# Optimization experiments

Hardware: AMD Instinct MI355X
Metric: run time of the kernel (lower is better)

Reference implementation:

```python
import jax, jax.numpy as jnp
import numpy as np

N = 50000      # nodes
E = 800000     # edges
T = 3          # npass
ED = 64        # embedding_dim
NS = 23        # nshifts (arange(0.8, 3.0+1e-5, 0.1))
MD = NS + ED   # message_dim = 87
H = 200        # hidden width (hardcoded in module)
NMOL = 2048    # number of molecules (segments for final scatter)
RD = ED * (T + 1)  # readout input dim = 256
EPS = 1e-5

SHIFTS = jnp.asarray(np.arange(0.8, 3.0 + 1e-5, 0.1, dtype=np.float32))  # [23]


def setup_inputs() -> dict:
    key = jax.random.key(0)
    ks = jax.random.split(key, 32)
    inp = {
        'z_i': jax.random.randint(ks[0], (N,), 0, 10),
        'edge_index': jax.random.randint(ks[1], (2, E), 0, N),
        'dist_ij': jax.random.uniform(ks[2], (E, 1), dtype=jnp.float32) * 2.2 + 0.8,
        'mol_ind': jnp.sort(jax.random.randint(ks[3], (N,), 0, NMOL)),
        'emb': jax.random.normal(ks[4], (10, ED), dtype=jnp.float32),
        # per-pass update MLP params, stacked over T
        'up_bn_g': jnp.ones((T, MD), jnp.float32),
        'up_bn_b': jnp.zeros((T, MD), jnp.float32),
        'up_w1': jax.random.normal(ks[5], (T, MD, H), jnp.float32) * 0.05,
        'up_b1': jnp.zeros((T, H), jnp.float32),
        'up_w2': jax.random.normal(ks[6], (T, H, H), jnp.float32) * 0.05,
        'up_b2': jnp.zeros((T, H), jnp.float32),
        'up_w3': jax.random.normal(ks[7], (T, H, H), jnp.float32) * 0.05,
        'up_b3': jnp.zeros((T, H), jnp.float32),
        'up_w4': jax.random.normal(ks[8], (T, H, ED), jnp.float32) * 0.05,
        'up_b4': jnp.zeros((T, ED), jnp.float32),
        # readout MLP params
        'ro_bn_g': jnp.ones((RD,), jnp.float32),
        'ro_bn_b': jnp.zeros((RD,), jnp.float32),
        'ro_w1': jax.random.normal(ks[9], (RD, H), jnp.float32) * 0.05,
        'ro_b1': jnp.zeros((H,), jnp.float32),
        'ro_w2': jax.random.normal(ks[10], (H, H), jnp.float32) * 0.05,
        'ro_b2': jnp.zeros((H,), jnp.float32),
        'ro_w3': jax.random.normal(ks[11], (H, H), jnp.float32) * 0.05,
        'ro_b3': jnp.zeros((H,), jnp.float32),
        'ro_w4': jax.random.normal(ks[12], (H, 1), jnp.float32) * 0.05,
        'ro_b4': jnp.zeros((1,), jnp.float32),  # bias filled to 0 in __init__
    }
    return inp


def batchnorm(x, g, b):
    # BatchNorm1d in training mode: batch statistics, biased variance
    mu = jnp.mean(x, axis=0)
    var = jnp.mean(jnp.square(x - mu), axis=0)
    return (x - mu) * jax.lax.rsqrt(var + EPS) * g + b


def mlp(x, g, b, w1, b1, w2, b2, w3, b3, w4, b4):
    x = batchnorm(x, g, b)
    x = jax.nn.relu(x @ w1 + b1)
    x = jax.nn.relu(x @ w2 + b2)
    x = jax.nn.relu(x @ w3 + b3)
    return x @ w4 + b4


def reference(z_i, edge_index, dist_ij, mol_ind, emb,
              up_bn_g, up_bn_b, up_w1, up_b1, up_w2, up_b2, up_w3, up_b3, up_w4, up_b4,
              ro_bn_g, ro_bn_b, ro_w1, ro_b1, ro_w2, ro_b2, ro_w3, ro_b3, ro_w4, ro_b4):
    e_source, e_sink = edge_index[0], edge_index[1]
    rbf_ij = jnp.exp(-jnp.square(dist_ij - SHIFTS[None, :]))  # [E, NS]
    x_i = emb[z_i]                                            # [N, ED]
    x_list = [x_i]
    for t in range(T):
        m_ij = jnp.concatenate([rbf_ij, x_i[e_sink]], axis=1)  # [E, MD] gather
        m_i = jax.ops.segment_sum(m_ij, e_source, num_segments=N)  # scatter-sum
        x_i = x_i + 0.1 * mlp(m_i, up_bn_g[t], up_bn_b[t],
                              up_w1[t], up_b1[t], up_w2[t], up_b2[t],
                              up_w3[t], up_b3[t], up_w4[t], up_b4[t])
        x_list.append(x_i)
    x_all = jnp.concatenate(x_list, axis=1)  # [N, RD]
    y_i = mlp(x_all, ro_bn_g, ro_bn_b, ro_w1, ro_b1, ro_w2, ro_b2, ro_w3, ro_b3, ro_w4, ro_b4)
    y = jax.ops.segment_sum(y_i, mol_ind, num_segments=NMOL)  # [NMOL, 1]
    return y
```

## Files before the change

### kernel.cpp

```cpp
#include <hip/hip_runtime.h>
#include <hip/hip_bf16.h>
#include <type_traits>

#define NN 50000
#define NP 50048
#define EE 800000
#define TT 3
#define ED 64
#define NS 23
#define MD 87
#define HH 200
#define NMOL 2048
#define RD 256

#define SW 216
#define NPB2 512
#define SNB ((NN + 255) / 256)

typedef __attribute__((ext_vector_type(8))) short short8b;
typedef __attribute__((ext_vector_type(4))) float f32x4;

template <int V> using ic = std::integral_constant<int, V>;

__device__ __forceinline__ unsigned short f2bf(float f) {
  unsigned u = __float_as_uint(f);
  return (unsigned short)((u + 0x7fffu + ((u >> 16) & 1u)) >> 16);
}
__device__ __forceinline__ float ubf2f(unsigned short h) {
  return __uint_as_float(((unsigned)h) << 16);
}
__device__ __forceinline__ float bfp2f(unsigned p) {
  return __uint_as_float(p << 16) + __uint_as_float(p & 0xffff0000u);
}
__device__ __forceinline__ unsigned packsplit(float v) {
  unsigned short h = f2bf(v);
  unsigned short l = f2bf(v - ubf2f(h));
  return (unsigned)h | ((unsigned)l << 16);
}

struct WD { const float* src; short* dst; int K, N, Kpad, Npad, T; };
struct WDs { WD d[5]; };

__global__ __launch_bounds__(256) void wprep_kernel(WDs W) {
  WD w = W.d[blockIdx.y];
  int KB = w.Kpad >> 5, NT = w.Npad >> 4;
  int per = w.Npad * w.Kpad;
  int total = w.T * per;
  for (int idx = blockIdx.x * 256 + threadIdx.x; idx < total; idx += gridDim.x * 256) {
    int t = idx / per;
    int r = idx - t * per;
    int e = r & 7, lane = (r >> 3) & 63;
    int blk = r >> 9;
    int kb = blk % KB, tile = blk / KB;
    int ln = lane & 15, quad = lane >> 4;
    int n = tile * 16 + ln, k = kb * 32 + quad * 8 + e;
    float v = 0.f;
    if (k < w.K && n < w.N) v = w.src[((size_t)t * w.K + k) * w.N + n];
    unsigned short h = f2bf(v);
    unsigned short l = f2bf(v - ubf2f(h));
    size_t base = ((size_t)(t * NT + tile) * KB + kb) * 1024;
    w.dst[base + lane * 8 + e] = (short)h;
    w.dst[base + 512 + lane * 8 + e] = (short)l;
  }
}

__global__ __launch_bounds__(256) void wscale_kernel(const float* __restrict__ wsrc,
                                                     const float* __restrict__ na,
                                                     const float* __restrict__ nb,
                                                     const float* __restrict__ bsrc,
                                                     int K, int Kpad,
                                                     short* __restrict__ wsp,
                                                     float* __restrict__ bc) {
  int n = blockIdx.x;
  int k = threadIdx.x;
  int KB = Kpad >> 5;
  int tile = n >> 4, ln = n & 15;
  float contrib = 0.f;
  if (k < Kpad) {
    float v = 0.f;
    if (n < HH && k < K) {
      float w = wsrc[(size_t)k * HH + n];
      v = na[k] * w;
      contrib = nb[k] * w;
    }
    unsigned short h = f2bf(v);
    unsigned short l = f2bf(v - ubf2f(h));
    int kb = k >> 5, quad = (k & 31) >> 3, e = k & 7;
    int lane = quad * 16 + ln;
    size_t base = ((size_t)tile * KB + kb) * 1024;
    wsp[base + lane * 8 + e] = (short)h;
    wsp[base + 512 + lane * 8 + e] = (short)l;
  }
  __shared__ float sh[256];
  sh[k] = contrib;
  __syncthreads();
  for (int off = 128; off > 0; off >>= 1) {
    if (k < off) sh[k] += sh[k + off];
    __syncthreads();
  }
  if (k == 0) bc[n] = (n < HH ? bsrc[n] : 0.f) + sh[0];
}

__global__ __launch_bounds__(256) void emb_kernel(const int* __restrict__ z,
                                                  const float* __restrict__ emb,
                                                  unsigned* __restrict__ xp,
                                                  short* __restrict__ xq,
                                                  short* __restrict__ xqs) {
  int idx = blockIdx.x * 256 + threadIdx.x;
  if (idx >= NN * ED) return;
  int i = idx >> 6, d = idx & 63;
  unsigned pk = packsplit(emb[z[i] * ED + d]);
  xp[(size_t)i * RD + d] = pk;
  short h = (short)(pk & 0xffffu);
  xq[(size_t)i * RD + d] = h;
  xqs[(size_t)i * ED + d] = h;
}

__global__ __launch_bounds__(256) void hist_kernel(const int* __restrict__ src,
                                                   int* __restrict__ deg) {
  int e = blockIdx.x * 256 + threadIdx.x;
  if (e < EE) atomicAdd(&deg[src[e]], 1);
}

__global__ __launch_bounds__(256) void scanA_kernel(const int* __restrict__ deg,
                                                    int* __restrict__ Psum) {
  int i = blockIdx.x * 256 + threadIdx.x;
  int v = (i < NN) ? deg[i] : 0;
#pragma unroll
  for (int off = 32; off > 0; off >>= 1) v += __shfl_down(v, off, 64);
  __shared__ int ws[4];
  if ((threadIdx.x & 63) == 0) ws[threadIdx.x >> 6] = v;
  __syncthreads();
  if (threadIdx.x == 0) Psum[blockIdx.x] = ws[0] + ws[1] + ws[2] + ws[3];
}

__global__ __launch_bounds__(256) void scanB_kernel(const int* __restrict__ Psum,
                                                    int* __restrict__ Poff) {
  __shared__ int sh[256];
  int t = threadIdx.x;
  int v = (t < SNB) ? Psum[t] : 0;
  sh[t] = v;
  __syncthreads();
  for (int off = 1; off < 256; off <<= 1) {
    int u = (t >= off) ? sh[t - off] : 0;
    __syncthreads();
    sh[t] += u;
    __syncthreads();
  }
  if (t < SNB) Poff[t] = sh[t] - v;
}

__global__ __launch_bounds__(256) void scanC_kernel(const int* __restrict__ deg,
                                                    const int* __restrict__ Poff,
                                                    int* __restrict__ offs,
                                                    int* __restrict__ cursor) {
  __shared__ int sh[256];
  int t = threadIdx.x;
  int i = blockIdx.x * 256 + t;
  int v = (i < NN) ? deg[i] : 0;
  sh[t] = v;
  __syncthreads();
  for (int off = 1; off < 256; off <<= 1) {
    int u = (t >= off) ? sh[t - off] : 0;
    __syncthreads();
    sh[t] += u;
    __syncthreads();
  }
  int excl = Poff[blockIdx.x] + sh[t] - v;
  if (i < NN) {
    offs[i] = excl;
    cursor[i] = excl;
    if (i == NN - 1) offs[NN] = excl + v;
  }
}

__global__ __launch_bounds__(256) void scatter_kernel(const int* __restrict__ src,
                                                      const int* __restrict__ snk,
                                                      const float* __restrict__ dist,
                                                      int* __restrict__ cursor,
                                                      int* __restrict__ ssink,
                                                      float* __restrict__ sdist) {
  int e = blockIdx.x * 256 + threadIdx.x;
  if (e >= EE) return;
  int p = atomicAdd(&cursor[src[e]], 1);
  ssink[p] = snk[e];
  sdist[p] = dist[e];
}

template <bool RBF>
__global__ __launch_bounds__(256) void gather_kernel(const int* __restrict__ offs,
                                                     const int* __restrict__ ssink,
                                                     const float* __restrict__ sdist,
                                                     const short* __restrict__ xqs,
                                                     short* __restrict__ mh) {
  int node = blockIdx.x * 4 + (threadIdx.x >> 6);
  int lane = threadIdx.x & 63;
  if (node >= NN) return;
  float shift = (float)(0.8 + 0.1 * (double)lane);
  int e0 = offs[node], e1 = offs[node + 1];
  float ax0 = 0.f, ax1 = 0.f, ar0 = 0.f, ar1 = 0.f;
  int j = e0;
  for (; j + 4 <= e1; j += 4) {
    int s0 = ssink[j], s1 = ssink[j + 1], s2 = ssink[j + 2], s3 = ssink[j + 3];
    float x0 = ubf2f((unsigned short)xqs[(size_t)s0 * ED + lane]);
    float x1 = ubf2f((unsigned short)xqs[(size_t)s1 * ED + lane]);
    float x2 = ubf2f((unsigned short)xqs[(size_t)s2 * ED + lane]);
    float x3 = ubf2f((unsigned short)xqs[(size_t)s3 * ED + lane]);
    ax0 += x0 + x2;
    ax1 += x1 + x3;
    if (RBF && lane < NS) {
      float d0 = sdist[j], d1 = sdist[j + 1], d2 = sdist[j + 2], d3 = sdist[j + 3];
      float u0 = d0 - shift, u1 = d1 - shift, u2 = d2 - shift, u3 = d3 - shift;
      ar0 += __expf(-u0 * u0) + __expf(-u2 * u2);
      ar1 += __expf(-u1 * u1) + __expf(-u3 * u3);
    }
  }
  for (; j < e1; j++) {
    int s = ssink[j];
    ax0 += ubf2f((unsigned short)xqs[(size_t)s * ED + lane]);
    if (RBF && lane < NS) {
      float u = sdist[j] - shift;
      ar0 += __expf(-u * u);
    }
  }
  float accx = ax0 + ax1;
  if (RBF && lane < NS) mh[(size_t)node * 96 + lane] = (short)f2bf(ar0 + ar1);
  if (RBF && lane >= NS && lane < 32) mh[(size_t)node * 96 + 64 + lane] = 0;
  mh[(size_t)node * 96 + NS + lane] = (short)f2bf(accx);
}

template <int LD>
__global__ __launch_bounds__(256) void colstats_s16_kernel(const short* __restrict__ X,
                                                           float* __restrict__ P) {
  constexpr int CG = LD / 8;
  constexpr int RPB = 256 / CG;
  const int t = threadIdx.x;
  const int cg = t % CG, rin = t / CG;
  float s[8] = {0, 0, 0, 0, 0, 0, 0, 0}, q[8] = {0, 0, 0, 0, 0, 0, 0, 0};
  if (rin < RPB) {
    for (int r = blockIdx.x * RPB + rin; r < NN; r += gridDim.x * RPB) {
      union { uint4 v; short e[8]; } u;
      u.v = *(const uint4*)(X + (size_t)r * LD + cg * 8);
#pragma unroll
      for (int e = 0; e < 8; e++) {
        float f = ubf2f((unsigned short)u.e[e]);
        s[e] += f;
        q[e] += f * f;
      }
    }
  }
  __shared__ float sh[256][16];
#pragma unroll
  for (int e = 0; e < 8; e++) { sh[t][e] = s[e]; sh[t][8 + e] = q[e]; }
  __syncthreads();
  if (rin == 0) {
    for (int rr = 1; rr < RPB; rr++) {
      const float* o = sh[rr * CG + cg];
#pragma unroll
      for (int e = 0; e < 8; e++) { s[e] += o[e]; q[e] += o[8 + e]; }
    }
    float* Pb = P + blockIdx.x * 512;
#pragma unroll
    for (int e = 0; e < 8; e++) {
      Pb[cg * 8 + e] = s[e];
      Pb[256 + cg * 8 + e] = q[e];
    }
  }
}

__global__ __launch_bounds__(256) void bnfinal2_kernel(const float* __restrict__ P, int nblk,
                                                       const float* __restrict__ g,
                                                       const float* __restrict__ b, int ncols,
                                                       float* __restrict__ na,
                                                       float* __restrict__ nb) {
  int c = blockIdx.x;
  int t = threadIdx.x;
  float s = 0.f, q = 0.f;
  for (int i = t; i < nblk; i += 256) {
    s += P[i * 512 + c];
    q += P[i * 512 + 256 + c];
  }
#pragma unroll
  for (int off = 32; off > 0; off >>= 1) {
    s += __shfl_down(s, off, 64);
    q += __shfl_down(q, off, 64);
  }
  __shared__ float ws[4], wq[4];
  if ((t & 63) == 0) { ws[t >> 6] = s; wq[t >> 6] = q; }
  __syncthreads();
  if (t == 0) {
    s = ws[0] + ws[1] + ws[2] + ws[3];
    q = wq[0] + wq[1] + wq[2] + wq[3];
    if (c < ncols) {
      float mean = s / (float)NN;
      float var = q / (float)NN - mean * mean;
      float a = g[c] * rsqrtf(var + 1e-5f);
      na[c] = a;
      nb[c] = b[c] - mean * a;
    } else {
      na[c] = 0.f;
      nb[c] = 0.f;
    }
  }
}

template <bool READOUT>
__global__ __launch_bounds__(256, 2) void fused_kernel(
    const short* __restrict__ Agh,
    const short* __restrict__ W1p, const short* __restrict__ W2p,
    const short* __restrict__ W3p, const short* __restrict__ W4p,
    const float* __restrict__ b1, const float* __restrict__ b2,
    const float* __restrict__ b3, const float* __restrict__ b4,
    unsigned* __restrict__ xp, short* __restrict__ xq, short* __restrict__ xqs,
    int t, const float* __restrict__ w4ro, const int* __restrict__ mol,
    float* __restrict__ out) {
  __shared__ short act[64 * SW];
  constexpr int GLDA = READOUT ? RD : 96;
  constexpr int KB1 = READOUT ? 8 : 3;
  constexpr int NB = READOUT ? 32 : 28;
  const int tid = threadIdx.x;
  const int wave = tid >> 6, lane = tid & 63, ln = lane & 15, quad = lane >> 4;
  const int q8 = quad * 8;
  const int bm = blockIdx.x * 64;

  *(unsigned*)(act + (tid >> 2) * SW + 208 + (tid & 3) * 2) = 0u;

  f32x4 acc[4][4];
  short8b Breg[NB];
  const short8b zfrag = {0, 0, 0, 0, 0, 0, 0, 0};

  auto loadB = [&](auto slt, auto tmt, auto ntt, const short* __restrict__ Wp,
                   int KBfull, int kb0) {
    constexpr int SL = decltype(slt)::value;
    constexpr int TM = decltype(tmt)::value;
    constexpr int NT = decltype(ntt)::value;
#pragma unroll
    for (int j = 0; j < 4; j++) {
      int tile = wave + 4 * j;
      if (tile < NT) {
#pragma unroll
        for (int s = 0; s < SL; s++) {
          int kb = kb0 + ((TM == 2) ? (s >> 1) : s);
          int pl = (TM == 2) ? ((s & 1) << 9) : 0;
          Breg[j * SL + s] = *(const short8b*)(
              Wp + (size_t)(tile * KBfull + kb) * 1024 + pl + lane * 8);
        }
      }
    }
    __builtin_amdgcn_sched_barrier(0);
  };

  auto mfmaloop = [&](auto slt, auto tmt, auto ntt, auto gat, auto rstt, int kb0) {
    constexpr int SL = decltype(slt)::value;
    constexpr int TM = decltype(tmt)::value;
    constexpr int NT = decltype(ntt)::value;
    constexpr bool GA = decltype(gat)::value;
    constexpr bool RST = decltype(rstt)::value;
    constexpr int KB = SL / TM;
    if constexpr (RST) {
#pragma unroll
      for (int j = 0; j < 4; j++)
#pragma unroll
        for (int i = 0; i < 4; i++) acc[j][i] = (f32x4){0.f, 0.f, 0.f, 0.f};
    }
#pragma unroll
    for (int kb = 0; kb < KB; kb++) {
      int col = (kb0 + kb) * 32 + q8;
      short8b a[4];
#pragma unroll
      for (int i = 0; i < 4; i++) {
        if constexpr (GA)
          a[i] = __builtin_nontemporal_load(
              (const short8b*)(Agh + (size_t)(bm + i * 16 + ln) * GLDA + col));
        else
          a[i] = (col < 216) ? *(const short8b*)(act + (i * 16 + ln) * SW + col)
                             : zfrag;
      }
#pragma unroll
      for (int s2 = 0; s2 < TM; s2++)
#pragma unroll
        for (int j = 0; j < 4; j++) {
          int tile = wave + 4 * j;
          if (tile < NT) {
#pragma unroll
            for (int i = 0; i < 4; i++)
              acc[j][i] = __builtin_amdgcn_mfma_f32_16x16x32_bf16(
                  a[i], Breg[j * SL + kb * TM + s2], acc[j][i], 0, 0, 0);
          }
        }
    }
  };

  auto epi = [&](const float* __restrict__ bias) {
#pragma unroll
    for (int j = 0; j < 4; j++) {
      int tile = wave + 4 * j;
      if (tile < 13) {
        int colg = tile * 16 + ln;
        float bb = (colg < HH) ? bias[colg] : 0.f;
#pragma unroll
        for (int i = 0; i < 4; i++)
#pragma unroll
          for (int r = 0; r < 4; r++)
            act[(i * 16 + quad * 4 + r) * SW + colg] =
                (short)f2bf(fmaxf(acc[j][i][r] + bb, 0.f));
      }
    }
  };

  auto bar = [] {
    __builtin_amdgcn_sched_barrier(0);
    __builtin_amdgcn_s_barrier();
    __builtin_amdgcn_sched_barrier(0);
  };
  auto lgkmbar = [] {
    asm volatile("s_waitcnt lgkmcnt(0)" ::: "memory");
    __builtin_amdgcn_sched_barrier(0);
    __builtin_amdgcn_s_barrier();
    __builtin_amdgcn_sched_barrier(0);
  };

  using T = std::true_type;
  using F = std::false_type;

  if constexpr (!READOUT) {
    loadB(ic<6>{}, ic<2>{}, ic<13>{}, W1p, KB1, 0);
    mfmaloop(ic<6>{}, ic<2>{}, ic<13>{}, T{}, T{}, 0);
  } else {
    loadB(ic<8>{}, ic<2>{}, ic<13>{}, W1p, KB1, 0);
    mfmaloop(ic<8>{}, ic<2>{}, ic<13>{}, T{}, T{}, 0);
    loadB(ic<8>{}, ic<2>{}, ic<13>{}, W1p, KB1, 4);
    mfmaloop(ic<8>{}, ic<2>{}, ic<13>{}, T{}, F{}, 4);
  }
  loadB(ic<7>{}, ic<1>{}, ic<13>{}, W2p, 7, 0);
  epi(b1);
  lgkmbar();

  mfmaloop(ic<7>{}, ic<1>{}, ic<13>{}, F{}, T{}, 0);
  loadB(ic<7>{}, ic<1>{}, ic<13>{}, W3p, 7, 0);
  bar();
  epi(b2);
  lgkmbar();

  mfmaloop(ic<7>{}, ic<1>{}, ic<13>{}, F{}, T{}, 0);
  if constexpr (!READOUT)
    loadB(ic<14>{}, ic<2>{}, ic<4>{}, W4p, 7, 0);
  bar();
  epi(b3);
  lgkmbar();

  if constexpr (!READOUT) {
    mfmaloop(ic<14>{}, ic<2>{}, ic<4>{}, F{}, T{}, 0);
    int colg = wave * 16 + ln;
    float bb = b4[colg];
#pragma unroll
    for (int i = 0; i < 4; i++)
#pragma unroll
      for (int r = 0; r < 4; r++) {
        int grow = bm + i * 16 + quad * 4 + r;
        if (grow < NN) {
          size_t base = (size_t)grow * RD;
          float oldv = bfp2f(xp[base + (size_t)t * ED + colg]);
          unsigned pk = packsplit(oldv + 0.1f * (acc[0][i][r] + bb));
          xp[base + (size_t)(t + 1) * ED + colg] = pk;
          short h = (short)(pk & 0xffffu);
          xq[base + (size_t)(t + 1) * ED + colg] = h;
          xqs[(size_t)(t + 1) * NN * ED + (size_t)grow * ED + colg] = h;
        }
      }
  } else {
    int row = tid >> 2;
    float s = 0.f;
    for (int c = (tid & 3); c < HH; c += 4)
      s += ubf2f((unsigned short)act[row * SW + c]) * w4ro[c];
    s += __shfl_xor(s, 1, 64);
    s += __shfl_xor(s, 2, 64);
    int grow = bm + row;
    if ((tid & 3) == 0 && grow < NN) atomicAdd(&out[mol[grow]], s + b4[0]);
  }
}

extern "C" void kernel_launch(void* const* d_in, const int* in_sizes, int n_in,
                              void* d_out, int out_size, void* d_ws, size_t ws_size,
                              hipStream_t stream) {
  const int* z_i = (const int*)d_in[0];
  const int* e_src = (const int*)d_in[1];
  const int* e_snk = ((const int*)d_in[1]) + EE;
  const float* dist = (const float*)d_in[2];
  const int* mol = (const int*)d_in[3];
  const float* emb = (const float*)d_in[4];
  const float* up_bn_g = (const float*)d_in[5];
  const float* up_bn_b = (const float*)d_in[6];
  const float* up_w1 = (const float*)d_in[7];
  const float* up_b1 = (const float*)d_in[8];
  const float* up_w2 = (const float*)d_in[9];
  const float* up_b2 = (const float*)d_in[10];
  const float* up_w3 = (const float*)d_in[11];
  const float* up_b3 = (const float*)d_in[12];
  const float* up_w4 = (const float*)d_in[13];
  const float* up_b4 = (const float*)d_in[14];
  const float* ro_bn_g = (const float*)d_in[15];
  const float* ro_bn_b = (const float*)d_in[16];
  const float* ro_w1 = (const float*)d_in[17];
  const float* ro_b1 = (const float*)d_in[18];
  const float* ro_w2 = (const float*)d_in[19];
  const float* ro_b2 = (const float*)d_in[20];
  const float* ro_w3 = (const float*)d_in[21];
  const float* ro_b3 = (const float*)d_in[22];
  const float* ro_w4 = (const float*)d_in[23];
  const float* ro_b4 = (const float*)d_in[24];
  float* out = (float*)d_out;

  char* p = (char*)d_ws;
  auto alloc = [&](size_t bytes) {
    void* r = (void*)p;
    p += (bytes + 255) & ~(size_t)255;
    return r;
  };
  unsigned* x_p = (unsigned*)alloc((size_t)NN * RD * 4);
  short* x_q = (short*)alloc((size_t)NP * RD * 2);
  short* x_qs = (short*)alloc((size_t)(TT + 1) * NN * ED * 2);
  short* mh = (short*)alloc((size_t)NP * 96 * 2);
  int* ssink = (int*)alloc((size_t)EE * 4);
  float* sdist = (float*)alloc((size_t)EE * 4);
  int* offs = (int*)alloc((size_t)(NN + 1) * 4);
  int* deg = (int*)alloc((size_t)NN * 4);
  int* cursor = (int*)alloc((size_t)NN * 4);
  int* Psum = (int*)alloc((size_t)SNB * 4);
  int* Poff = (int*)alloc((size_t)SNB * 4);
  float* P = (float*)alloc((size_t)NPB2 * 512 * 4);
  float* na = (float*)alloc(256 * 4);
  float* nb = (float*)alloc(256 * 4);
  float* b1c = (float*)alloc(208 * 4);
  short* w1sp = (short*)alloc((size_t)13 * 3 * 1024 * 2);
  short* r1sp = (short*)alloc((size_t)13 * 8 * 1024 * 2);
  short* w2p = (short*)alloc((size_t)TT * 13 * 7 * 1024 * 2);
  short* w3p = (short*)alloc((size_t)TT * 13 * 7 * 1024 * 2);
  short* w4p = (short*)alloc((size_t)TT * 4 * 7 * 1024 * 2);
  short* r2p = (short*)alloc((size_t)13 * 7 * 1024 * 2);
  short* r3p = (short*)alloc((size_t)13 * 7 * 1024 * 2);

  hipMemsetAsync(deg, 0, (size_t)NN * 4, stream);
  hipMemsetAsync(out, 0, (size_t)NMOL * 4, stream);

  WDs descs;
  descs.d[0] = {up_w2, w2p, HH, HH, 224, 208, TT};
  descs.d[1] = {up_w3, w3p, HH, HH, 224, 208, TT};
  descs.d[2] = {up_w4, w4p, HH, ED, 224, 64, TT};
  descs.d[3] = {ro_w2, r2p, HH, HH, 224, 208, 1};
  descs.d[4] = {ro_w3, r3p, HH, HH, 224, 208, 1};
  wprep_kernel<<<dim3(546, 5), 256, 0, stream>>>(descs);

  emb_kernel<<<(NN * ED + 255) / 256, 256, 0, stream>>>(z_i, emb, x_p, x_q, x_qs);
  hist_kernel<<<(EE + 255) / 256, 256, 0, stream>>>(e_src, deg);
  scanA_kernel<<<SNB, 256, 0, stream>>>(deg, Psum);
  scanB_kernel<<<1, 256, 0, stream>>>(Psum, Poff);
  scanC_kernel<<<SNB, 256, 0, stream>>>(deg, Poff, offs, cursor);
  scatter_kernel<<<(EE + 255) / 256, 256, 0, stream>>>(e_src, e_snk, dist, cursor, ssink, sdist);

  const int gM = NP / 64;

  for (int t = 0; t < TT; t++) {
    if (t == 0)
      gather_kernel<true><<<(NN + 3) / 4, 256, 0, stream>>>(
          offs, ssink, sdist, x_qs, mh);
    else
      gather_kernel<false><<<(NN + 3) / 4, 256, 0, stream>>>(
          offs, ssink, sdist, x_qs + (size_t)t * NN * ED, mh);
    colstats_s16_kernel<96><<<NPB2, 256, 0, stream>>>(mh, P);
    bnfinal2_kernel<<<256, 256, 0, stream>>>(P, NPB2, up_bn_g + t * MD, up_bn_b + t * MD, MD,
                                             na, nb);
    wscale_kernel<<<208, 256, 0, stream>>>(up_w1 + (size_t)t * MD * HH, na, nb,
                                           up_b1 + t * HH, MD, 96, w1sp, b1c);
    fused_kernel<false><<<gM, 256, 0, stream>>>(
        mh, w1sp,
        w2p + (size_t)t * 13 * 7 * 1024, w3p + (size_t)t * 13 * 7 * 1024,
        w4p + (size_t)t * 4 * 7 * 1024,
        b1c, up_b2 + t * HH, up_b3 + t * HH, up_b4 + t * ED,
        x_p, x_q, x_qs, t, nullptr, nullptr, nullptr);
  }

  colstats_s16_kernel<256><<<NPB2, 256, 0, stream>>>(x_q, P);
  bnfinal2_kernel<<<256, 256, 0, stream>>>(P, NPB2, ro_bn_g, ro_bn_b, RD, na, nb);
  wscale_kernel<<<208, 256, 0, stream>>>(ro_w1, na, nb, ro_b1, RD, 256, r1sp, b1c);
  fused_kernel<true><<<gM, 256, 0, stream>>>(
      x_q, r1sp, r2p, r3p, nullptr,
      b1c, ro_b2, ro_b3, ro_b4,
      nullptr, nullptr, nullptr, 0, ro_w4, mol, out);

  (void)in_sizes; (void)n_in; (void)out_size; (void)ws_size;
}
```

Baseline: 555.0 us.

## Fuse batchnorm column statistics into producer kernels and drop separate stats passes

Column sum and sum-of-squares for the batchnorm inputs are now accumulated inside the gather, embedding, and fused MLP kernels via shared-memory reductions and global atomics. The mean/scale computation is folded into the weight-scaling kernel, which removes the colstats and bnfinal kernels and their extra reads of the message and feature matrices. The gather and embedding kernels become grid-stride with a fixed grid size. In exchange, the change adds atomic contention, per-pass memsets, and float-atomic ordering nondeterminism in the statistics.

```diff
diff --git a/kernel.cpp b/kernel.cpp
--- a/kernel.cpp
+++ b/kernel.cpp
@@ -14,7 +14,6 @@
 #define RD 256
 
 #define SW 216
-#define NPB2 512
 #define SNB ((NN + 255) / 256)
 
 typedef __attribute__((ext_vector_type(8))) short short8b;
@@ -64,13 +63,15 @@
   }
 }
 
-__global__ __launch_bounds__(256) void wscale_kernel(const float* __restrict__ wsrc,
-                                                     const float* __restrict__ na,
-                                                     const float* __restrict__ nb,
-                                                     const float* __restrict__ bsrc,
-                                                     int K, int Kpad,
-                                                     short* __restrict__ wsp,
-                                                     float* __restrict__ bc) {
+__global__ __launch_bounds__(256) void wscale2_kernel(const float* __restrict__ wsrc,
+                                                      const float* __restrict__ g,
+                                                      const float* __restrict__ bvec,
+                                                      const float* __restrict__ bsrc,
+                                                      const float* __restrict__ s0,
+                                                      const float* __restrict__ s1,
+                                                      int SPLIT, int K, int Kpad,
+                                                      short* __restrict__ wsp,
+                                                      float* __restrict__ bc) {
   int n = blockIdx.x;
   int k = threadIdx.x;
   int KB = Kpad >> 5;
@@ -79,9 +80,17 @@
   if (k < Kpad) {
     float v = 0.f;
     if (n < HH && k < K) {
+      float sum, sq;
+      if (k < SPLIT) { sum = s0[k]; sq = s0[256 + k]; }
+      else           { sum = s1[k - SPLIT]; sq = s1[256 + k - SPLIT]; }
+      const float inv = 1.f / (float)NN;
+      float mean = sum * inv;
+      float var = sq * inv - mean * mean;
+      float a = g[k] * rsqrtf(var + 1e-5f);
+      float nbv = bvec[k] - mean * a;
       float w = wsrc[(size_t)k * HH + n];
-      v = na[k] * w;
-      contrib = nb[k] * w;
+      v = a * w;
+      contrib = nbv * w;
     }
     unsigned short h = f2bf(v);
     unsigned short l = f2bf(v - ubf2f(h));
@@ -105,15 +114,31 @@
                                                   const float* __restrict__ emb,
                                                   unsigned* __restrict__ xp,
                                                   short* __restrict__ xq,
-                                                  short* __restrict__ xqs) {
-  int idx = blockIdx.x * 256 + threadIdx.x;
-  if (idx >= NN * ED) return;
-  int i = idx >> 6, d = idx & 63;
-  unsigned pk = packsplit(emb[z[i] * ED + d]);
-  xp[(size_t)i * RD + d] = pk;
-  short h = (short)(pk & 0xffffu);
-  xq[(size_t)i * RD + d] = h;
-  xqs[(size_t)i * ED + d] = h;
+                                                  short* __restrict__ xqs,
+                                                  float* __restrict__ xsS) {
+  const int tid = threadIdx.x;
+  float sx = 0.f, sxx = 0.f;
+  for (int idx = blockIdx.x * 256 + tid; idx < NN * ED; idx += gridDim.x * 256) {
+    int i = idx >> 6, d = idx & 63;
+    unsigned pk = packsplit(emb[z[i] * ED + d]);
+    xp[(size_t)i * RD + d] = pk;
+    short h = (short)(pk & 0xffffu);
+    xq[(size_t)i * RD + d] = h;
+    xqs[(size_t)i * ED + d] = h;
+    float f = ubf2f((unsigned short)h);
+    sx += f;
+    sxx += f * f;
+  }
+  __shared__ float ls[256], lq[256];
+  ls[tid] = sx;
+  lq[tid] = sxx;
+  __syncthreads();
+  if (tid < 64) {
+    float a = ls[tid] + ls[tid + 64] + ls[tid + 128] + ls[tid + 192];
+    float b = lq[tid] + lq[tid + 64] + lq[tid + 128] + lq[tid + 192];
+    atomicAdd(&xsS[tid], a);
+    atomicAdd(&xsS[256 + tid], b);
+  }
 }
 
 __global__ __launch_bounds__(256) void hist_kernel(const int* __restrict__ src,
@@ -192,114 +217,75 @@
                                                      const int* __restrict__ ssink,
                                                      const float* __restrict__ sdist,
                                                      const short* __restrict__ xqs,
-                                                     short* __restrict__ mh) {
-  int node = blockIdx.x * 4 + (threadIdx.x >> 6);
-  int lane = threadIdx.x & 63;
-  if (node >= NN) return;
+                                                     short* __restrict__ mh,
+                                                     float* __restrict__ mxS,
+                                                     float* __restrict__ rbfS) {
+  const int lane = threadIdx.x & 63, w = threadIdx.x >> 6;
   float shift = (float)(0.8 + 0.1 * (double)lane);
-  int e0 = offs[node], e1 = offs[node + 1];
-  float ax0 = 0.f, ax1 = 0.f, ar0 = 0.f, ar1 = 0.f;
-  int j = e0;
-  for (; j + 4 <= e1; j += 4) {
-    int s0 = ssink[j], s1 = ssink[j + 1], s2 = ssink[j + 2], s3 = ssink[j + 3];
-    float x0 = ubf2f((unsigned short)xqs[(size_t)s0 * ED + lane]);
-    float x1 = ubf2f((unsigned short)xqs[(size_t)s1 * ED + lane]);
-    float x2 = ubf2f((unsigned short)xqs[(size_t)s2 * ED + lane]);
-    float x3 = ubf2f((unsigned short)xqs[(size_t)s3 * ED + lane]);
-    ax0 += x0 + x2;
-    ax1 += x1 + x3;
-    if (RBF && lane < NS) {
-      float d0 = sdist[j], d1 = sdist[j + 1], d2 = sdist[j + 2], d3 = sdist[j + 3];
-      float u0 = d0 - shift, u1 = d1 - shift, u2 = d2 - shift, u3 = d3 - shift;
-      ar0 += __expf(-u0 * u0) + __expf(-u2 * u2);
-      ar1 += __expf(-u1 * u1) + __expf(-u3 * u3);
-    }
-  }
-  for (; j < e1; j++) {
-    int s = ssink[j];
-    ax0 += ubf2f((unsigned short)xqs[(size_t)s * ED + lane]);
-    if (RBF && lane < NS) {
-      float u = sdist[j] - shift;
-      ar0 += __expf(-u * u);
-    }
-  }
-  float accx = ax0 + ax1;
-  if (RBF && lane < NS) mh[(size_t)node * 96 + lane] = (short)f2bf(ar0 + ar1);
-  if (RBF && lane >= NS && lane < 32) mh[(size_t)node * 96 + 64 + lane] = 0;
-  mh[(size_t)node * 96 + NS + lane] = (short)f2bf(accx);
-}
-
-template <int LD>
-__global__ __launch_bounds__(256) void colstats_s16_kernel(const short* __restrict__ X,
-                                                           float* __restrict__ P) {
-  constexpr int CG = LD / 8;
-  constexpr int RPB = 256 / CG;
-  const int t = threadIdx.x;
-  const int cg = t % CG, rin = t / CG;
-  float s[8] = {0, 0, 0, 0, 0, 0, 0, 0}, q[8] = {0, 0, 0, 0, 0, 0, 0, 0};
-  if (rin < RPB) {
-    for (int r = blockIdx.x * RPB + rin; r < NN; r += gridDim.x * RPB) {
-      union { uint4 v; short e[8]; } u;
-      u.v = *(const uint4*)(X + (size_t)r * LD + cg * 8);
-#pragma unroll
-      for (int e = 0; e < 8; e++) {
-        float f = ubf2f((unsigned short)u.e[e]);
-        s[e] += f;
-        q[e] += f * f;
-      }
-    }
-  }
-  __shared__ float sh[256][16];
-#pragma unroll
-  for (int e = 0; e < 8; e++) { sh[t][e] = s[e]; sh[t][8 + e] = q[e]; }
+  float sx = 0.f, sxx = 0.f, sr = 0.f, srr = 0.f;
+  for (int node = blockIdx.x * 4 + w; node < NN; node += gridDim.x * 4) {
+    int e0 = offs[node], e1 = offs[node + 1];
+    float ax0 = 0.f, ax1 = 0.f, ar0 = 0.f, ar1 = 0.f;
+    int j = e0;
+    for (; j + 4 <= e1; j += 4) {
+      int s0 = ssink[j], s1 = ssink[j + 1], s2 = ssink[j + 2], s3 = ssink[j + 3];
+      float x0 = ubf2f((unsigned short)xqs[(size_t)s0 * ED + lane]);
+      float x1 = ubf2f((unsigned short)xqs[(size_t)s1 * ED + lane]);
+      float x2 = ubf2f((unsigned short)xqs[(size_t)s2 * ED + lane]);
+      float x3 = ubf2f((unsigned short)xqs[(size_t)s3 * ED + lane]);
+      ax0 += x0 + x2;
+      ax1 += x1 + x3;
+      if (RBF && lane < NS) {
+        float d0 = sdist[j], d1 = sdist[j + 1], d2 = sdist[j + 2], d3 = sdist[j + 3];
+        float u0 = d0 - shift, u1 = d1 - shift, u2 = d2 - shift, u3 = d3 - shift;
+        ar0 += __expf(-u0 * u0) + __expf(-u2 * u2);
+        ar1 += __expf(-u1 * u1) + __expf(-u3 * u3);
+      }
+    }
+    for (; j < e1; j++) {
+      int s = ssink[j];
+      ax0 += ubf2f((unsigned short)xqs[(size_t)s * ED + lane]);
+      if (RBF && lane < NS) {
+        float u = sdist[j] - shift;
+        ar0 += __expf(-u * u);
+      }
+    }
+    unsigned short hx = f2bf(ax0 + ax1);
+    mh[(size_t)node * 96 + NS + lane] = (short)hx;
+    float fx = ubf2f(hx);
+    sx += fx;
+    sxx += fx * fx;
+    if (RBF) {
+      if (lane < NS) {
+        unsigned short hr = f2bf(ar0 + ar1);
+        mh[(size_t)node * 96 + lane] = (short)hr;
+        float fr = ubf2f(hr);
+        sr += fr;
+        srr += fr * fr;
+      }
+      if (lane >= NS && lane < 32) mh[(size_t)node * 96 + 64 + lane] = 0;
+    }
+  }
+  __shared__ float ls[4][64], lq[4][64];
+  ls[w][lane] = sx;
+  lq[w][lane] = sxx;
   __syncthreads();
-  if (rin == 0) {
-    for (int rr = 1; rr < RPB; rr++) {
-      const float* o = sh[rr * CG + cg];
-#pragma unroll
-      for (int e = 0; e < 8; e++) { s[e] += o[e]; q[e] += o[8 + e]; }
-    }
-    float* Pb = P + blockIdx.x * 512;
-#pragma unroll
-    for (int e = 0; e < 8; e++) {
-      Pb[cg * 8 + e] = s[e];
-      Pb[256 + cg * 8 + e] = q[e];
-    }
-  }
-}
-
-__global__ __launch_bounds__(256) void bnfinal2_kernel(const float* __restrict__ P, int nblk,
-                                                       const float* __restrict__ g,
-                                                       const float* __restrict__ b, int ncols,
-                                                       float* __restrict__ na,
-                                                       float* __restrict__ nb) {
-  int c = blockIdx.x;
-  int t = threadIdx.x;
-  float s = 0.f, q = 0.f;
-  for (int i = t; i < nblk; i += 256) {
-    s += P[i * 512 + c];
-    q += P[i * 512 + 256 + c];
-  }
-#pragma unroll
-  for (int off = 32; off > 0; off >>= 1) {
-    s += __shfl_down(s, off, 64);
-    q += __shfl_down(q, off, 64);
-  }
-  __shared__ float ws[4], wq[4];
-  if ((t & 63) == 0) { ws[t >> 6] = s; wq[t >> 6] = q; }
-  __syncthreads();
-  if (t == 0) {
-    s = ws[0] + ws[1] + ws[2] + ws[3];
-    q = wq[0] + wq[1] + wq[2] + wq[3];
-    if (c < ncols) {
-      float mean = s / (float)NN;
-      float var = q / (float)NN - mean * mean;
-      float a = g[c] * rsqrtf(var + 1e-5f);
-      na[c] = a;
-      nb[c] = b[c] - mean * a;
-    } else {
-      na[c] = 0.f;
-      nb[c] = 0.f;
+  if (w == 0) {
+    float a = ls[0][lane] + ls[1][lane] + ls[2][lane] + ls[3][lane];
+    float b = lq[0][lane] + lq[1][lane] + lq[2][lane] + lq[3][lane];
+    atomicAdd(&mxS[lane], a);
+    atomicAdd(&mxS[256 + lane], b);
+  }
+  if (RBF) {
+    __syncthreads();
+    ls[w][lane] = sr;
+    lq[w][lane] = srr;
+    __syncthreads();
+    if (w == 0 && lane < NS) {
+      float a = ls[0][lane] + ls[1][lane] + ls[2][lane] + ls[3][lane];
+      float b = lq[0][lane] + lq[1][lane] + lq[2][lane] + lq[3][lane];
+      atomicAdd(&rbfS[lane], a);
+      atomicAdd(&rbfS[256 + lane], b);
     }
   }
 }
@@ -313,7 +299,7 @@
     const float* __restrict__ b3, const float* __restrict__ b4,
     unsigned* __restrict__ xp, short* __restrict__ xq, short* __restrict__ xqs,
     int t, const float* __restrict__ w4ro, const int* __restrict__ mol,
-    float* __restrict__ out) {
+    float* __restrict__ out, float* __restrict__ xsS) {
   __shared__ short act[64 * SW];
   constexpr int GLDA = READOUT ? RD : 96;
   constexpr int KB1 = READOUT ? 8 : 3;
@@ -453,6 +439,7 @@
     mfmaloop(ic<14>{}, ic<2>{}, ic<4>{}, F{}, T{}, 0);
     int colg = wave * 16 + ln;
     float bb = b4[colg];
+    float sx = 0.f, sxx = 0.f;
 #pragma unroll
     for (int i = 0; i < 4; i++)
 #pragma unroll
@@ -466,8 +453,19 @@
           short h = (short)(pk & 0xffffu);
           xq[base + (size_t)(t + 1) * ED + colg] = h;
           xqs[(size_t)(t + 1) * NN * ED + (size_t)grow * ED + colg] = h;
+          float f = ubf2f((unsigned short)h);
+          sx += f;
+          sxx += f * f;
         }
       }
+    sx += __shfl_xor(sx, 16, 64);
+    sx += __shfl_xor(sx, 32, 64);
+    sxx += __shfl_xor(sxx, 16, 64);
+    sxx += __shfl_xor(sxx, 32, 64);
+    if (quad == 0) {
+      atomicAdd(&xsS[(t + 1) * ED + colg], sx);
+      atomicAdd(&xsS[256 + (t + 1) * ED + colg], sxx);
+    }
   } else {
     int row = tid >> 2;
     float s = 0.f;
@@ -528,9 +526,9 @@
   int* cursor = (int*)alloc((size_t)NN * 4);
   int* Psum = (int*)alloc((size_t)SNB * 4);
   int* Poff = (int*)alloc((size_t)SNB * 4);
-  float* P = (float*)alloc((size_t)NPB2 * 512 * 4);
-  float* na = (float*)alloc(256 * 4);
-  float* nb = (float*)alloc(256 * 4);
+  float* mxS = (float*)alloc(512 * 4);
+  float* rbfS = (float*)alloc(512 * 4);
+  float* xsS = (float*)alloc(512 * 4);
   float* b1c = (float*)alloc(208 * 4);
   short* w1sp = (short*)alloc((size_t)13 * 3 * 1024 * 2);
   short* r1sp = (short*)alloc((size_t)13 * 8 * 1024 * 2);
@@ -542,6 +540,8 @@
 
   hipMemsetAsync(deg, 0, (size_t)NN * 4, stream);
   hipMemsetAsync(out, 0, (size_t)NMOL * 4, stream);
+  hipMemsetAsync(rbfS, 0, 512 * 4, stream);
+  hipMemsetAsync(xsS, 0, 512 * 4, stream);
 
   WDs descs;
   descs.d[0] = {up_w2, w2p, HH, HH, 224, 208, TT};
@@ -551,7 +551,7 @@
   descs.d[4] = {ro_w3, r3p, HH, HH, 224, 208, 1};
   wprep_kernel<<<dim3(546, 5), 256, 0, stream>>>(descs);
 
-  emb_kernel<<<(NN * ED + 255) / 256, 256, 0, stream>>>(z_i, emb, x_p, x_q, x_qs);
+  emb_kernel<<<1024, 256, 0, stream>>>(z_i, emb, x_p, x_q, x_qs, xsS);
   hist_kernel<<<(EE + 255) / 256, 256, 0, stream>>>(e_src, deg);
   scanA_kernel<<<SNB, 256, 0, stream>>>(deg, Psum);
   scanB_kernel<<<1, 256, 0, stream>>>(Psum, Poff);
@@ -561,32 +561,31 @@
   const int gM = NP / 64;
 
   for (int t = 0; t < TT; t++) {
+    hipMemsetAsync(mxS, 0, 512 * 4, stream);
     if (t == 0)
-      gather_kernel<true><<<(NN + 3) / 4, 256, 0, stream>>>(
-          offs, ssink, sdist, x_qs, mh);
+      gather_kernel<true><<<1024, 256, 0, stream>>>(
+          offs, ssink, sdist, x_qs, mh, mxS, rbfS);
     else
-      gather_kernel<false><<<(NN + 3) / 4, 256, 0, stream>>>(
-          offs, ssink, sdist, x_qs + (size_t)t * NN * ED, mh);
-    colstats_s16_kernel<96><<<NPB2, 256, 0, stream>>>(mh, P);
-    bnfinal2_kernel<<<256, 256, 0, stream>>>(P, NPB2, up_bn_g + t * MD, up_bn_b + t * MD, MD,
-                                             na, nb);
-    wscale_kernel<<<208, 256, 0, stream>>>(up_w1 + (size_t)t * MD * HH, na, nb,
-                                           up_b1 + t * HH, MD, 96, w1sp, b1c);
+      gather_kernel<false><<<1024, 256, 0, stream>>>(
+          offs, ssink, sdist, x_qs + (size_t)t * NN * ED, mh, mxS, rbfS);
+    wscale2_kernel<<<208, 256, 0, stream>>>(up_w1 + (size_t)t * MD * HH,
+                                            up_bn_g + t * MD, up_bn_b + t * MD,
+                                            up_b1 + t * HH, rbfS, mxS, NS, MD, 96,
+                                            w1sp, b1c);
     fused_kernel<false><<<gM, 256, 0, stream>>>(
         mh, w1sp,
         w2p + (size_t)t * 13 * 7 * 1024, w3p + (size_t)t * 13 * 7 * 1024,
         w4p + (size_t)t * 4 * 7 * 1024,
         b1c, up_b2 + t * HH, up_b3 + t * HH, up_b4 + t * ED,
-        x_p, x_q, x_qs, t, nullptr, nullptr, nullptr);
-  }
-
-  colstats_s16_kernel<256><<<NPB2, 256, 0, stream>>>(x_q, P);
-  bnfinal2_kernel<<<256, 256, 0, stream>>>(P, NPB2, ro_bn_g, ro_bn_b, RD, na, nb);
-  wscale_kernel<<<208, 256, 0, stream>>>(ro_w1, na, nb, ro_b1, RD, 256, r1sp, b1c);
+        x_p, x_q, x_qs, t, nullptr, nullptr, nullptr, xsS);
+  }
+
+  wscale2_kernel<<<208, 256, 0, stream>>>(ro_w1, ro_bn_g, ro_bn_b, ro_b1,
+                                          xsS, xsS, 0, RD, 256, r1sp, b1c);
   fused_kernel<true><<<gM, 256, 0, stream>>>(
       x_q, r1sp, r2p, r3p, nullptr,
       b1c, ro_b2, ro_b3, ro_b4,
-      nullptr, nullptr, nullptr, 0, ro_w4, mol, out);
+      nullptr, nullptr, nullptr, 0, ro_w4, mol, out, nullptr);
 
   (void)in_sizes; (void)n_in; (void)out_size; (void)ws_size;
 }
```

Result: slower. 694.6 us (+25.1%).

## Fuse readout batchnorm column statistics into update epilogue atomics

Applied to the files above, without the earlier changes.

Computes per-column sum and sum-of-squares of the readout input inside each pass's fused update epilogue, plus one small kernel for the embedding slice, accumulating with atomics. This replaces the separate column-stats pass over the 50000x256 readout input and the bnfinal kernel. A new wscale2 kernel derives the batchnorm scale and shift directly from those sums. The trade-off is extra atomic traffic and float atomic ordering nondeterminism, and variance is now computed as E[x^2]-mean^2 in fp32.

```diff
diff --git a/kernel.cpp b/kernel.cpp
--- a/kernel.cpp
+++ b/kernel.cpp
@@ -101,6 +101,49 @@
   if (k == 0) bc[n] = (n < HH ? bsrc[n] : 0.f) + sh[0];
 }
 
+__global__ __launch_bounds__(256) void wscale2_kernel(const float* __restrict__ wsrc,
+                                                      const float* __restrict__ g,
+                                                      const float* __restrict__ bvec,
+                                                      const float* __restrict__ bsrc,
+                                                      const float* __restrict__ s,
+                                                      int K, int Kpad,
+                                                      short* __restrict__ wsp,
+                                                      float* __restrict__ bc) {
+  int n = blockIdx.x;
+  int k = threadIdx.x;
+  int KB = Kpad >> 5;
+  int tile = n >> 4, ln = n & 15;
+  float contrib = 0.f;
+  if (k < Kpad) {
+    float v = 0.f;
+    if (n < HH && k < K) {
+      const float inv = 1.f / (float)NN;
+      float mean = s[k] * inv;
+      float var = s[256 + k] * inv - mean * mean;
+      float a = g[k] * rsqrtf(var + 1e-5f);
+      float nbv = bvec[k] - mean * a;
+      float w = wsrc[(size_t)k * HH + n];
+      v = a * w;
+      contrib = nbv * w;
+    }
+    unsigned short h = f2bf(v);
+    unsigned short l = f2bf(v - ubf2f(h));
+    int kb = k >> 5, quad = (k & 31) >> 3, e = k & 7;
+    int lane = quad * 16 + ln;
+    size_t base = ((size_t)tile * KB + kb) * 1024;
+    wsp[base + lane * 8 + e] = (short)h;
+    wsp[base + 512 + lane * 8 + e] = (short)l;
+  }
+  __shared__ float sh[256];
+  sh[k] = contrib;
+  __syncthreads();
+  for (int off = 128; off > 0; off >>= 1) {
+    if (k < off) sh[k] += sh[k + off];
+    __syncthreads();
+  }
+  if (k == 0) bc[n] = (n < HH ? bsrc[n] : 0.f) + sh[0];
+}
+
 __global__ __launch_bounds__(256) void emb_kernel(const int* __restrict__ z,
                                                   const float* __restrict__ emb,
                                                   unsigned* __restrict__ xp,
@@ -114,6 +157,27 @@
   short h = (short)(pk & 0xffffu);
   xq[(size_t)i * RD + d] = h;
   xqs[(size_t)i * ED + d] = h;
+}
+
+__global__ __launch_bounds__(256) void slice0stats_kernel(const short* __restrict__ xqs,
+                                                          float* __restrict__ xsS) {
+  const int tid = threadIdx.x;
+  float sx = 0.f, sxx = 0.f;
+  for (int idx = blockIdx.x * 256 + tid; idx < NN * ED; idx += gridDim.x * 256) {
+    float f = ubf2f((unsigned short)xqs[idx]);
+    sx += f;
+    sxx += f * f;
+  }
+  __shared__ float ls[256], lq[256];
+  ls[tid] = sx;
+  lq[tid] = sxx;
+  __syncthreads();
+  if (tid < 64) {
+    float a = ls[tid] + ls[tid + 64] + ls[tid + 128] + ls[tid + 192];
+    float b = lq[tid] + lq[tid + 64] + lq[tid + 128] + lq[tid + 192];
+    atomicAdd(&xsS[tid], a);
+    atomicAdd(&xsS[256 + tid], b);
+  }
 }
 
 __global__ __launch_bounds__(256) void hist_kernel(const int* __restrict__ src,
@@ -313,7 +377,7 @@
     const float* __restrict__ b3, const float* __restrict__ b4,
     unsigned* __restrict__ xp, short* __restrict__ xq, short* __restrict__ xqs,
     int t, const float* __restrict__ w4ro, const int* __restrict__ mol,
-    float* __restrict__ out) {
+    float* __restrict__ out, float* __restrict__ xsS) {
   __shared__ short act[64 * SW];
   constexpr int GLDA = READOUT ? RD : 96;
   constexpr int KB1 = READOUT ? 8 : 3;
@@ -453,6 +517,7 @@
     mfmaloop(ic<14>{}, ic<2>{}, ic<4>{}, F{}, T{}, 0);
     int colg = wave * 16 + ln;
     float bb = b4[colg];
+    float sx = 0.f, sxx = 0.f;
 #pragma unroll
     for (int i = 0; i < 4; i++)
 #pragma unroll
@@ -466,8 +531,19 @@
           short h = (short)(pk & 0xffffu);
           xq[base + (size_t)(t + 1) * ED + colg] = h;
           xqs[(size_t)(t + 1) * NN * ED + (size_t)grow * ED + colg] = h;
+          float f = ubf2f((unsigned short)h);
+          sx += f;
+          sxx += f * f;
         }
       }
+    sx += __shfl_xor(sx, 16, 64);
+    sx += __shfl_xor(sx, 32, 64);
+    sxx += __shfl_xor(sxx, 16, 64);
+    sxx += __shfl_xor(sxx, 32, 64);
+    if (quad == 0) {
+      atomicAdd(&xsS[(t + 1) * ED + colg], sx);
+      atomicAdd(&xsS[256 + (t + 1) * ED + colg], sxx);
+    }
   } else {
     int row = tid >> 2;
     float s = 0.f;
@@ -531,6 +607,7 @@
   float* P = (float*)alloc((size_t)NPB2 * 512 * 4);
   float* na = (float*)alloc(256 * 4);
   float* nb = (float*)alloc(256 * 4);
+  float* xsS = (float*)alloc(512 * 4);
   float* b1c = (float*)alloc(208 * 4);
   short* w1sp = (short*)alloc((size_t)13 * 3 * 1024 * 2);
   short* r1sp = (short*)alloc((size_t)13 * 8 * 1024 * 2);
@@ -542,6 +619,7 @@
 
   hipMemsetAsync(deg, 0, (size_t)NN * 4, stream);
   hipMemsetAsync(out, 0, (size_t)NMOL * 4, stream);
+  hipMemsetAsync(xsS, 0, 512 * 4, stream);
 
   WDs descs;
   descs.d[0] = {up_w2, w2p, HH, HH, 224, 208, TT};
@@ -552,6 +630,7 @@
   wprep_kernel<<<dim3(546, 5), 256, 0, stream>>>(descs);
 
   emb_kernel<<<(NN * ED + 255) / 256, 256, 0, stream>>>(z_i, emb, x_p, x_q, x_qs);
+  slice0stats_kernel<<<512, 256, 0, stream>>>(x_qs, xsS);
   hist_kernel<<<(EE + 255) / 256, 256, 0, stream>>>(e_src, deg);
   scanA_kernel<<<SNB, 256, 0, stream>>>(deg, Psum);
   scanB_kernel<<<1, 256, 0, stream>>>(Psum, Poff);
@@ -577,16 +656,15 @@
         w2p + (size_t)t * 13 * 7 * 1024, w3p + (size_t)t * 13 * 7 * 1024,
         w4p + (size_t)t * 4 * 7 * 1024,
         b1c, up_b2 + t * HH, up_b3 + t * HH, up_b4 + t * ED,
-        x_p, x_q, x_qs, t, nullptr, nullptr, nullptr);
-  }
-
-  colstats_s16_kernel<256><<<NPB2, 256, 0, stream>>>(x_q, P);
-  bnfinal2_kernel<<<256, 256, 0, stream>>>(P, NPB2, ro_bn_g, ro_bn_b, RD, na, nb);
-  wscale_kernel<<<208, 256, 0, stream>>>(ro_w1, na, nb, ro_b1, RD, 256, r1sp, b1c);
+        x_p, x_q, x_qs, t, nullptr, nullptr, nullptr, xsS);
+  }
+
+  wscale2_kernel<<<208, 256, 0, stream>>>(ro_w1, ro_bn_g, ro_bn_b, ro_b1,
+                                          xsS, RD, 256, r1sp, b1c);
   fused_kernel<true><<<gM, 256, 0, stream>>>(
       x_q, r1sp, r2p, r3p, nullptr,
       b1c, ro_b2, ro_b3, ro_b4,
-      nullptr, nullptr, nullptr, 0, ro_w4, mol, out);
+      nullptr, nullptr, nullptr, 0, ro_w4, mol, out, nullptr);
 
   (void)in_sizes; (void)n_in; (void)out_size; (void)ws_size;
 }
```

After: 601.7 us. 8.4% more time.
